# Kernel tuning notes

Measured on AMD Instinct MI355X. Metric: run time of the kernel, lower is better.

The kernel has to match this reference:

```python
import jax, jax.numpy as jnp
import numpy as np

N, C, HH, WW = 16, 512, 64, 96
FEAT_STRIDE = 16
RATIOS = (0.5, 1.0, 2.0)
SCALES = (8.0, 16.0, 32.0)
BASE = 16.0
NA = len(RATIOS) * len(SCALES)  # 9 anchors per location


def _anchor_base():
    py = px = BASE / 2.0
    rows = []
    for r in RATIOS:
        for s in SCALES:
            h = BASE * s * np.sqrt(r)
            w = BASE * s * np.sqrt(1.0 / r)
            rows.append([py - h / 2.0, px - w / 2.0, py + h / 2.0, px + w / 2.0])
    return np.asarray(rows, dtype=np.float32)


def _shifted_anchors(hh, ww):
    # mirrors enumerate_shifted_anchor body (which lacks a return in the source)
    ab = _anchor_base()
    y = np.arange(hh, dtype=np.float32) * FEAT_STRIDE
    x = np.arange(ww, dtype=np.float32) * FEAT_STRIDE
    mx, my = np.meshgrid(x, y)
    shift = np.stack([my.ravel(), mx.ravel(), my.ravel(), mx.ravel()], axis=1)
    return (shift[:, None, :] + ab[None, :, :]).reshape(-1, 4).astype(np.float32)


def setup_inputs() -> dict:
    key = jax.random.key(0)
    ks = jax.random.split(key, 3)
    x = jax.random.normal(ks[0], (N, C, HH, WW), dtype=jnp.float32)
    # small init scale keeps softmax unsaturated (512-dim contraction)
    loc_w = jax.random.normal(ks[1], (NA * 4, C), dtype=jnp.float32) * 0.01
    loc_b = jnp.zeros((NA * 4,), dtype=jnp.float32)
    score_w = jax.random.normal(ks[2], (NA * 2, C), dtype=jnp.float32) * 0.01
    score_b = jnp.zeros((NA * 2,), dtype=jnp.float32)
    return {"x": x, "loc_w": loc_w, "loc_b": loc_b, "score_w": score_w, "score_b": score_b}


def reference(x, loc_w, loc_b, score_w, score_b):
    n, _, hh, ww = x.shape
    anchor = jnp.asarray(_shifted_anchors(hh, ww))  # (hh*ww*NA, 4)
    # NOTE: source computes h = relu(conv1(x)) but then applies loc/score to x
    # (h is dead code), so the faithful reference applies the 1x1 convs to x.
    # 1x1 conv == channel contraction; permute(0,2,3,1) folded into einsum output order.
    rpn_loc = jnp.einsum('nchw,oc->nhwo', x, loc_w) + loc_b          # (n, hh, ww, 36)
    rpn_loc = rpn_loc.reshape(n, -1, 4)                               # (n, hh*ww*NA, 4)
    rpn_score = jnp.einsum('nchw,oc->nhwo', x, score_w) + score_b    # (n, hh, ww, 18)
    sm = jax.nn.softmax(rpn_score.reshape(n, hh, ww, NA, 2), axis=-1)
    rpn_fg_scores = sm[..., 1].reshape(n, -1)                         # (n, hh*ww*NA)
    return rpn_loc, rpn_score, rpn_fg_scores, anchor
```

## Files before the change

kernel.cpp:

```cpp
#include <hip/hip_runtime.h>
#include <hip/hip_bf16.h>
#include <math.h>

#define CC 512
#define HH 64
#define WW 96
#define NN 16
#define HW (HH*WW)
#define NA 9
#define NLOC 36
#define NSC 18
#define NO_PAD 64

typedef __attribute__((ext_vector_type(4))) float f32x4;
typedef __attribute__((ext_vector_type(2))) float f32x2;
typedef __attribute__((ext_vector_type(8))) short s16x8;

__device__ __forceinline__ unsigned short f2bf(float f) {
    __hip_bfloat16 h = __float2bfloat16(f);
    union { __hip_bfloat16 h; unsigned short u; } cv;
    cv.h = h;
    return cv.u;
}
__device__ __forceinline__ unsigned pk2(float lo, float hi) {
    return (unsigned)f2bf(lo) | ((unsigned)f2bf(hi) << 16);
}

__global__ void prep_w_kernel(const float* __restrict__ lw,
                              const float* __restrict__ sw,
                              unsigned short* __restrict__ wbf) {
    int i = blockIdx.x * 256 + threadIdx.x;
    if (i >= NO_PAD * CC) return;
    int o = i >> 9, c = i & 511;
    float v = 0.0f;
    if (o < NLOC) v = lw[o * CC + c];
    else if (o < 54) v = sw[(o - NLOC) * CC + c];
    wbf[i] = f2bf(v);
}

__launch_bounds__(256, 3)
__global__ void rpn_mfma_kernel(const float* __restrict__ x,
                                const unsigned short* __restrict__ wbf,
                                const float* __restrict__ lb,
                                const float* __restrict__ sb,
                                float* __restrict__ out0,
                                float* __restrict__ out1,
                                float* __restrict__ out2,
                                float* __restrict__ out3) {
    const int tid  = threadIdx.x;
    const int lane = tid & 63;
    const int w    = tid >> 6;
    const int col  = lane & 15;
    const int rgrp = lane >> 4;
    const int krow = rgrp * 8;

    const int bid  = blockIdx.x;
    const int swz  = (bid & 7) * 96 + (bid >> 3);
    const int pbase = swz * 128;
    const int n     = pbase / HW;
    const int rem   = pbase % HW;
    const float* xA = x + (size_t)n * CC * HW + rem + w * 32 + 2 * col;
    const unsigned short* wB = wbf + (size_t)col * CC + krow;

    f32x4 acc0[4], acc1[4];
    #pragma unroll
    for (int nt = 0; nt < 4; ++nt) {
        acc0[nt] = (f32x4){0.f, 0.f, 0.f, 0.f};
        acc1[nt] = (f32x4){0.f, 0.f, 0.f, 0.f};
    }

    f32x2 aA[8], aB[8];
    s16x8 bA[4], bB[4];

    #pragma unroll
    for (int j = 0; j < 8; ++j)
        aA[j] = *reinterpret_cast<const f32x2*>(xA + (size_t)(krow + j) * HW);
    #pragma unroll
    for (int nt = 0; nt < 4; ++nt)
        bA[nt] = *reinterpret_cast<const s16x8*>(wB + (size_t)nt * 16 * CC);

    #pragma unroll 1
    for (int ks = 0; ks < 16; ks += 2) {
        const int kb1 = (ks + 1) * 32;
        const int kb2 = (ks + 2) * 32;

        #pragma unroll
        for (int j = 0; j < 8; ++j)
            aB[j] = *reinterpret_cast<const f32x2*>(
                xA + (size_t)(kb1 + krow + j) * HW);
        #pragma unroll
        for (int nt = 0; nt < 4; ++nt)
            bB[nt] = *reinterpret_cast<const s16x8*>(
                wB + (size_t)nt * 16 * CC + kb1);

        {
            union { unsigned u[4]; s16x8 v; } fa0, fa1;
            #pragma unroll
            for (int j = 0; j < 4; ++j) {
                fa0.u[j] = pk2(aA[2 * j].x, aA[2 * j + 1].x);
                fa1.u[j] = pk2(aA[2 * j].y, aA[2 * j + 1].y);
            }
            #pragma unroll
            for (int nt = 0; nt < 4; ++nt)
                acc0[nt] = __builtin_amdgcn_mfma_f32_16x16x32_bf16(fa0.v, bA[nt], acc0[nt], 0, 0, 0);
            #pragma unroll
            for (int nt = 0; nt < 4; ++nt)
                acc1[nt] = __builtin_amdgcn_mfma_f32_16x16x32_bf16(fa1.v, bA[nt], acc1[nt], 0, 0, 0);
        }

        if (ks < 14) {
            #pragma unroll
            for (int j = 0; j < 8; ++j)
                aA[j] = *reinterpret_cast<const f32x2*>(
                    xA + (size_t)(kb2 + krow + j) * HW);
            #pragma unroll
            for (int nt = 0; nt < 4; ++nt)
                bA[nt] = *reinterpret_cast<const s16x8*>(
                    wB + (size_t)nt * 16 * CC + kb2);
        }

        {
            union { unsigned u[4]; s16x8 v; } fa0, fa1;
            #pragma unroll
            for (int j = 0; j < 4; ++j) {
                fa0.u[j] = pk2(aB[2 * j].x, aB[2 * j + 1].x);
                fa1.u[j] = pk2(aB[2 * j].y, aB[2 * j + 1].y);
            }
            #pragma unroll
            for (int nt = 0; nt < 4; ++nt)
                acc0[nt] = __builtin_amdgcn_mfma_f32_16x16x32_bf16(fa0.v, bB[nt], acc0[nt], 0, 0, 0);
            #pragma unroll
            for (int nt = 0; nt < 4; ++nt)
                acc1[nt] = __builtin_amdgcn_mfma_f32_16x16x32_bf16(fa1.v, bB[nt], acc1[nt], 0, 0, 0);
        }
    }

    #pragma unroll
    for (int m = 0; m < 2; ++m) {
        #pragma unroll
        for (int nt = 0; nt < 4; ++nt) {
            int o = nt * 16 + col;
            float bias = (o < NLOC) ? lb[o] : ((o < 54) ? sb[o - NLOC] : 0.0f);
            #pragma unroll
            for (int r = 0; r < 4; ++r) {
                float val  = (m == 0 ? acc0[nt][r] : acc1[nt][r]) + bias;
                float part = __shfl_xor(val, 1);
                int pgl = pbase + w * 32 + 2 * (rgrp * 4 + r) + m;
                if (o < NLOC) {
                    out0[(size_t)pgl * NLOC + o] = val;
                } else if (o < 54) {
                    int os = o - NLOC;
                    out1[(size_t)pgl * NSC + os] = val;
                    if ((os & 1) == 0)
                        out2[(size_t)pgl * NA + (os >> 1)] = 1.0f / (1.0f + __expf(val - part));
                }
            }
        }
    }

    if (tid < 72) {
        int t = bid * 72 + tid;
        int a9   = t % NA;
        int rem2 = t / NA;
        int h = rem2 / WW, ww2 = rem2 % WW;
        int ri = a9 / 3, si = a9 % 3;
        const double ratios[3] = {0.5, 1.0, 2.0};
        const double scales[3] = {8.0, 16.0, 32.0};
        double ha = 16.0 * scales[si] * sqrt(ratios[ri]);
        double wa = 16.0 * scales[si] * sqrt(1.0 / ratios[ri]);
        float y1 = (float)(8.0 - ha * 0.5);
        float x1 = (float)(8.0 - wa * 0.5);
        float y2 = (float)(8.0 + ha * 0.5);
        float x2 = (float)(8.0 + wa * 0.5);
        float sy = (float)(h * 16);
        float sx = (float)(ww2 * 16);
        float4 v = make_float4(sy + y1, sx + x1, sy + y2, sx + x2);
        *reinterpret_cast<float4*>(out3 + (size_t)t * 4) = v;
    }
}

extern "C" void kernel_launch(void* const* d_in, const int* in_sizes, int n_in,
                              void* d_out, int out_size, void* d_ws, size_t ws_size,
                              hipStream_t stream) {
    const float* x  = (const float*)d_in[0];
    const float* lw = (const float*)d_in[1];
    const float* lb = (const float*)d_in[2];
    const float* sw = (const float*)d_in[3];
    const float* sb = (const float*)d_in[4];

    float* out0 = (float*)d_out;
    float* out1 = out0 + (size_t)NN * HW * NLOC;
    float* out2 = out1 + (size_t)NN * HW * NSC;
    float* out3 = out2 + (size_t)NN * HW * NA;

    unsigned short* wbf = (unsigned short*)d_ws;

    int grid_w = (NO_PAD * CC + 255) / 256;
    prep_w_kernel<<<grid_w, 256, 0, stream>>>(lw, sw, wbf);

    int grid_m = NN * HW / 128;
    rpn_mfma_kernel<<<grid_m, 256, 0, stream>>>(x, wbf, lb, sb, out0, out1, out2, out3);
}
```

Baseline: 50.86 us.

## Halve per-block pixel tile to 64 and double grid for occupancy

Each block now covers 64 pixels instead of 128. Each wave loads one scalar float per channel row instead of a float2 pair, and keeps one accumulator set instead of two. The grid doubles, and launch bounds move to 5 blocks per CU so more waves can be resident to hide global-load latency on the streaming x read. In exchange, every weight fragment is reloaded twice as often per pixel, global loads become narrower, and each MFMA round has less ILP.

```diff
diff --git a/kernel.cpp b/kernel.cpp
--- a/kernel.cpp
+++ b/kernel.cpp
@@ -13,7 +13,6 @@
 #define NO_PAD 64
 
 typedef __attribute__((ext_vector_type(4))) float f32x4;
-typedef __attribute__((ext_vector_type(2))) float f32x2;
 typedef __attribute__((ext_vector_type(8))) short s16x8;
 
 __device__ __forceinline__ unsigned short f2bf(float f) {
@@ -38,7 +37,7 @@
     wbf[i] = f2bf(v);
 }
 
-__launch_bounds__(256, 3)
+__launch_bounds__(256, 5)
 __global__ void rpn_mfma_kernel(const float* __restrict__ x,
                                 const unsigned short* __restrict__ wbf,
                                 const float* __restrict__ lb,
@@ -55,26 +54,23 @@
     const int krow = rgrp * 8;
 
     const int bid  = blockIdx.x;
-    const int swz  = (bid & 7) * 96 + (bid >> 3);
-    const int pbase = swz * 128;
+    const int swz  = (bid & 7) * 192 + (bid >> 3);
+    const int pbase = swz * 64;
     const int n     = pbase / HW;
     const int rem   = pbase % HW;
-    const float* xA = x + (size_t)n * CC * HW + rem + w * 32 + 2 * col;
+    const float* xA = x + (size_t)n * CC * HW + rem + w * 16 + col;
     const unsigned short* wB = wbf + (size_t)col * CC + krow;
 
-    f32x4 acc0[4], acc1[4];
+    f32x4 acc[4];
     #pragma unroll
-    for (int nt = 0; nt < 4; ++nt) {
-        acc0[nt] = (f32x4){0.f, 0.f, 0.f, 0.f};
-        acc1[nt] = (f32x4){0.f, 0.f, 0.f, 0.f};
-    }
+    for (int nt = 0; nt < 4; ++nt) acc[nt] = (f32x4){0.f, 0.f, 0.f, 0.f};
 
-    f32x2 aA[8], aB[8];
+    float aA[8], aB[8];
     s16x8 bA[4], bB[4];
 
     #pragma unroll
     for (int j = 0; j < 8; ++j)
-        aA[j] = *reinterpret_cast<const f32x2*>(xA + (size_t)(krow + j) * HW);
+        aA[j] = xA[(size_t)(krow + j) * HW];
     #pragma unroll
     for (int nt = 0; nt < 4; ++nt)
         bA[nt] = *reinterpret_cast<const s16x8*>(wB + (size_t)nt * 16 * CC);
@@ -86,33 +82,25 @@
 
         #pragma unroll
         for (int j = 0; j < 8; ++j)
-            aB[j] = *reinterpret_cast<const f32x2*>(
-                xA + (size_t)(kb1 + krow + j) * HW);
+            aB[j] = xA[(size_t)(kb1 + krow + j) * HW];
         #pragma unroll
         for (int nt = 0; nt < 4; ++nt)
             bB[nt] = *reinterpret_cast<const s16x8*>(
                 wB + (size_t)nt * 16 * CC + kb1);
 
         {
-            union { unsigned u[4]; s16x8 v; } fa0, fa1;
+            union { unsigned u[4]; s16x8 v; } fa;
             #pragma unroll
-            for (int j = 0; j < 4; ++j) {
-                fa0.u[j] = pk2(aA[2 * j].x, aA[2 * j + 1].x);
-                fa1.u[j] = pk2(aA[2 * j].y, aA[2 * j + 1].y);
-            }
+            for (int j = 0; j < 4; ++j) fa.u[j] = pk2(aA[2 * j], aA[2 * j + 1]);
             #pragma unroll
             for (int nt = 0; nt < 4; ++nt)
-                acc0[nt] = __builtin_amdgcn_mfma_f32_16x16x32_bf16(fa0.v, bA[nt], acc0[nt], 0, 0, 0);
-            #pragma unroll
-            for (int nt = 0; nt < 4; ++nt)
-                acc1[nt] = __builtin_amdgcn_mfma_f32_16x16x32_bf16(fa1.v, bA[nt], acc1[nt], 0, 0, 0);
+                acc[nt] = __builtin_amdgcn_mfma_f32_16x16x32_bf16(fa.v, bA[nt], acc[nt], 0, 0, 0);
         }
 
         if (ks < 14) {
             #pragma unroll
             for (int j = 0; j < 8; ++j)
-                aA[j] = *reinterpret_cast<const f32x2*>(
-                    xA + (size_t)(kb2 + krow + j) * HW);
+                aA[j] = xA[(size_t)(kb2 + krow + j) * HW];
             #pragma unroll
             for (int nt = 0; nt < 4; ++nt)
                 bA[nt] = *reinterpret_cast<const s16x8*>(
@@ -120,46 +108,37 @@
         }
 
         {
-            union { unsigned u[4]; s16x8 v; } fa0, fa1;
+            union { unsigned u[4]; s16x8 v; } fa;
             #pragma unroll
-            for (int j = 0; j < 4; ++j) {
-                fa0.u[j] = pk2(aB[2 * j].x, aB[2 * j + 1].x);
-                fa1.u[j] = pk2(aB[2 * j].y, aB[2 * j + 1].y);
-            }
+            for (int j = 0; j < 4; ++j) fa.u[j] = pk2(aB[2 * j], aB[2 * j + 1]);
             #pragma unroll
             for (int nt = 0; nt < 4; ++nt)
-                acc0[nt] = __builtin_amdgcn_mfma_f32_16x16x32_bf16(fa0.v, bB[nt], acc0[nt], 0, 0, 0);
-            #pragma unroll
-            for (int nt = 0; nt < 4; ++nt)
-                acc1[nt] = __builtin_amdgcn_mfma_f32_16x16x32_bf16(fa1.v, bB[nt], acc1[nt], 0, 0, 0);
+                acc[nt] = __builtin_amdgcn_mfma_f32_16x16x32_bf16(fa.v, bB[nt], acc[nt], 0, 0, 0);
         }
     }
 
     #pragma unroll
-    for (int m = 0; m < 2; ++m) {
+    for (int nt = 0; nt < 4; ++nt) {
+        int o = nt * 16 + col;
+        float bias = (o < NLOC) ? lb[o] : ((o < 54) ? sb[o - NLOC] : 0.0f);
         #pragma unroll
-        for (int nt = 0; nt < 4; ++nt) {
-            int o = nt * 16 + col;
-            float bias = (o < NLOC) ? lb[o] : ((o < 54) ? sb[o - NLOC] : 0.0f);
-            #pragma unroll
-            for (int r = 0; r < 4; ++r) {
-                float val  = (m == 0 ? acc0[nt][r] : acc1[nt][r]) + bias;
-                float part = __shfl_xor(val, 1);
-                int pgl = pbase + w * 32 + 2 * (rgrp * 4 + r) + m;
-                if (o < NLOC) {
-                    out0[(size_t)pgl * NLOC + o] = val;
-                } else if (o < 54) {
-                    int os = o - NLOC;
-                    out1[(size_t)pgl * NSC + os] = val;
-                    if ((os & 1) == 0)
-                        out2[(size_t)pgl * NA + (os >> 1)] = 1.0f / (1.0f + __expf(val - part));
-                }
+        for (int r = 0; r < 4; ++r) {
+            float val  = acc[nt][r] + bias;
+            float part = __shfl_xor(val, 1);
+            int p = pbase + w * 16 + rgrp * 4 + r;
+            if (o < NLOC) {
+                out0[(size_t)p * NLOC + o] = val;
+            } else if (o < 54) {
+                int os = o - NLOC;
+                out1[(size_t)p * NSC + os] = val;
+                if ((os & 1) == 0)
+                    out2[(size_t)p * NA + (os >> 1)] = 1.0f / (1.0f + __expf(val - part));
             }
         }
     }
 
-    if (tid < 72) {
-        int t = bid * 72 + tid;
+    if (tid < 36) {
+        int t = bid * 36 + tid;
         int a9   = t % NA;
         int rem2 = t / NA;
         int h = rem2 / WW, ww2 = rem2 % WW;
@@ -198,6 +177,6 @@
     int grid_w = (NO_PAD * CC + 255) / 256;
     prep_w_kernel<<<grid_w, 256, 0, stream>>>(lw, sw, wbf);
 
-    int grid_m = NN * HW / 128;
+    int grid_m = NN * HW / 64;
     rpn_mfma_kernel<<<grid_m, 256, 0, stream>>>(x, wbf, lb, sb, out0, out1, out2, out3);
 }
```

Result: slower. 68.49 us (+34.7%).
